# Performance work log

Hardware: AMD Instinct MI355X
Metric: run time of the kernel (lower is better)

Reference implementation:

```python
import jax, jax.numpy as jnp
import numpy as np

NUM_EXPERTS = 64
TOP_K = 2
NOISE_EPS = 0.01


def setup_inputs() -> dict:
    key = jax.random.key(0)
    k1, k2, k3, k4 = jax.random.split(key, 4)
    B, D, E = 32768, 2048, NUM_EXPERTS
    x = jax.random.normal(k1, (B, D), dtype=jnp.float32)
    # original inits these to zero; use small random weights for a non-degenerate top-k
    w_gate = jax.random.normal(k2, (D, E), dtype=jnp.float32) * 0.02
    w_noise = jax.random.normal(k3, (D, E), dtype=jnp.float32) * 0.02
    noise = jax.random.normal(k4, (B, E), dtype=jnp.float32)  # tf.random.normal draw, fixed
    return {"x": x, "w_gate": w_gate, "w_noise": w_noise, "noise": noise}


def reference(x, w_gate, w_noise, noise):
    # routing_pooling='flatten' on a 2D input is identity
    pooled = x  # [B, D]
    routing = pooled @ w_gate  # [B, E]
    # noisy routing (training=True path)
    noise_stddev = jax.nn.softplus(pooled @ w_noise) + NOISE_EPS
    routing = routing + noise * noise_stddev
    # softmax_top_k: take top k+1, keep top k, softmax, scatter back to E experts
    kk = min(TOP_K + 1, NUM_EXPERTS)
    top_vals, top_idx = jax.lax.top_k(routing, kk)
    top_k_vals = top_vals[:, :TOP_K]            # [B, k]
    top_k_idx = top_idx[:, :TOP_K]              # [B, k]
    top_k_gates = jax.nn.softmax(top_k_vals, axis=-1)
    B = routing.shape[0]
    rows = jnp.arange(B)[:, None]
    # rowwise_unsorted_segment_sum -> scatter gates into expert slots
    out = jnp.zeros((B, NUM_EXPERTS), dtype=routing.dtype).at[rows, top_k_idx].add(top_k_gates)
    return out
```

## Files before the change

kernel.cpp:

```cpp
#include <hip/hip_runtime.h>
#include <math.h>


typedef _Float16 half8v __attribute__((ext_vector_type(8)));
typedef float f32x4  __attribute__((ext_vector_type(4)));
typedef float f32x16 __attribute__((ext_vector_type(16)));

constexpr int DIMK = 2048;
constexpr int NEXP = 64;
constexpr int BM   = 64;
constexpr int NCH  = DIMK / 32;

__device__ __forceinline__ void async_load16(const void* g, void* l) {
    __builtin_amdgcn_global_load_lds(
        (const __attribute__((address_space(1))) unsigned int*)g,
        (__attribute__((address_space(3))) unsigned int*)l, 16, 0, 0);
}

__device__ __forceinline__ bool gt_pair(float a, int ia, float b, int ib) {
    return (a > b) || (a == b && ia < ib);
}

__global__ __launch_bounds__(256)
void presplit_kernel(const float* __restrict__ wg, const float* __restrict__ wn,
                     _Float16* __restrict__ wsB)
{
    int gid  = blockIdx.x * 256 + threadIdx.x;
    int lane = gid & 63;
    int fb   = gid >> 6;
    int nt   = fb & 3;
    int p    = (fb >> 2) & 1;
    int kh   = (fb >> 3) & 1;
    int c    = fb >> 4;
    const float* src = (nt < 2) ? (wg + nt * 32 + (lane & 31))
                                : (wn + (nt - 2) * 32 + (lane & 31));
    int kb = c * 32 + kh * 16 + ((lane >> 5) << 3);
    half8v hp;
    #pragma unroll
    for (int j = 0; j < 8; ++j) {
        float w = src[(size_t)(kb + j) * NEXP] * 65536.0f;
        _Float16 a = (_Float16)w;
        hp[j] = p ? (_Float16)(w - (float)a) : a;
    }
    *(half8v*)(wsB + (size_t)fb * 512 + lane * 8) = hp;
}

__global__ __launch_bounds__(256, 2)
void routing_mfma(const float* __restrict__ x, const _Float16* __restrict__ wsB,
                  const float* __restrict__ noise, float* __restrict__ out)
{
    __shared__ _Float16 Bp[4][16][64][8];
    __shared__ float4   cand[BM][2];
    __shared__ float4   res[BM];

    const int tid  = threadIdx.x;
    const int lane = tid & 63;
    const int w    = tid >> 6;
    const int rg   = w >> 1;
    const int colh = w & 1;
    const int m    = lane & 31;
    const int h    = lane >> 5;
    const int row0 = blockIdx.x * BM;

    f32x16 acc[2] = {};
    float4 ra[4][4];
    half8v afH[2][2], afL[2][2];

    const float* xp = x + (size_t)(row0 + rg * 32 + m) * DIMK + h * 8;

    auto issue_B = [&](int c, int buf) {
        #pragma unroll
        for (int ii = 0; ii < 4; ++ii) {
            int idx = w * 4 + ii;
            const _Float16* g = wsB + ((size_t)c * 16 + idx) * 512 + lane * 8;
            async_load16(g, &Bp[buf][idx][0][0]);
        }
    };

#define ISSUE_X(C, S)                                            \
    {   const float* p_ = xp + (C) * 32;                         \
        ra[S][0] = *(const float4*)(p_);                         \
        ra[S][1] = *(const float4*)(p_ + 4);                     \
        ra[S][2] = *(const float4*)(p_ + 16);                    \
        ra[S][3] = *(const float4*)(p_ + 20);  }

#define CONVERT(C, P)                                                        \
    {   _Pragma("unroll")                                                    \
        for (int kh = 0; kh < 2; ++kh) {                                     \
            float4 u = ra[(C) & 3][kh * 2];                                  \
            float4 v = ra[(C) & 3][kh * 2 + 1];                              \
            float f0 = u.x * 1024.f, f1 = u.y * 1024.f;                      \
            float f2 = u.z * 1024.f, f3 = u.w * 1024.f;                      \
            float f4 = v.x * 1024.f, f5 = v.y * 1024.f;                      \
            float f6 = v.z * 1024.f, f7 = v.w * 1024.f;                      \
            _Float16 a0=(_Float16)f0, a1=(_Float16)f1, a2=(_Float16)f2,      \
                     a3=(_Float16)f3, a4=(_Float16)f4, a5=(_Float16)f5,      \
                     a6=(_Float16)f6, a7=(_Float16)f7;                       \
            afH[P][kh][0]=a0; afH[P][kh][1]=a1; afH[P][kh][2]=a2;            \
            afH[P][kh][3]=a3; afH[P][kh][4]=a4; afH[P][kh][5]=a5;            \
            afH[P][kh][6]=a6; afH[P][kh][7]=a7;                             \
            afL[P][kh][0]=(_Float16)(f0-(float)a0);                         \
            afL[P][kh][1]=(_Float16)(f1-(float)a1);                         \
            afL[P][kh][2]=(_Float16)(f2-(float)a2);                         \
            afL[P][kh][3]=(_Float16)(f3-(float)a3);                         \
            afL[P][kh][4]=(_Float16)(f4-(float)a4);                         \
            afL[P][kh][5]=(_Float16)(f5-(float)a5);                         \
            afL[P][kh][6]=(_Float16)(f6-(float)a6);                         \
            afL[P][kh][7]=(_Float16)(f7-(float)a7);                         \
        }                                                                    \
    }

#define FENCE() asm volatile("" ::: "memory")

#define STEP(T, ISS, CV, WN)                                                 \
    {                                                                        \
        asm volatile("s_waitcnt vmcnt(" #WN ")" ::: "memory");               \
        asm volatile("s_barrier" ::: "memory");                              \
        if (ISS) { issue_B((T) + 2, ((T) + 2) & 3);                          \
                   ISSUE_X((T) + 2, ((T) + 2) & 3); }                        \
        half8v bf[2][2][2];                                                  \
        _Pragma("unroll")                                                    \
        for (int kh = 0; kh < 2; ++kh)                                       \
            _Pragma("unroll")                                                \
            for (int p = 0; p < 2; ++p)                                      \
                _Pragma("unroll")                                            \
                for (int tl = 0; tl < 2; ++tl)                               \
                    bf[kh][p][tl] = *(const half8v*)                         \
                        &Bp[(T) & 3][kh * 8 + p * 4 + tl * 2 + colh][lane][0];\
        __builtin_amdgcn_s_setprio(1);                                       \
        _Pragma("unroll")                                                    \
        for (int tl = 0; tl < 2; ++tl)                                       \
            _Pragma("unroll")                                                \
            for (int kh = 0; kh < 2; ++kh) {                                 \
                acc[tl] = __builtin_amdgcn_mfma_f32_32x32x16_f16(            \
                    afH[(T) & 1][kh], bf[kh][0][tl], acc[tl], 0, 0, 0);      \
                acc[tl] = __builtin_amdgcn_mfma_f32_32x32x16_f16(            \
                    afH[(T) & 1][kh], bf[kh][1][tl], acc[tl], 0, 0, 0);      \
                acc[tl] = __builtin_amdgcn_mfma_f32_32x32x16_f16(            \
                    afL[(T) & 1][kh], bf[kh][0][tl], acc[tl], 0, 0, 0);      \
            }                                                                \
        __builtin_amdgcn_s_setprio(0);                                       \
        if (CV) CONVERT((T) + 1, ((T) + 1) & 1);                             \
    }

    issue_B(0, 0);
    ISSUE_X(0, 0);
    FENCE();
    issue_B(1, 1);
    ISSUE_X(1, 1);
    CONVERT(0, 0);

    #pragma unroll 1
    for (int t = 0; t < NCH - 4; t += 4) {
        STEP(t + 0, 1, 1, 8)
        STEP(t + 1, 1, 1, 8)
        STEP(t + 2, 1, 1, 8)
        STEP(t + 3, 1, 1, 8)
    }
    STEP(NCH - 4, 1, 1, 8)
    STEP(NCH - 3, 1, 1, 8)
    STEP(NCH - 2, 0, 1, 8)
    STEP(NCH - 1, 0, 0, 0)

#undef STEP
#undef CONVERT
#undef ISSUE_X
#undef FENCE

    const float s = 0x1p-26f;
    {
        const int e = colh * 32 + m;
        #pragma unroll
        for (int reg = 0; reg < 16; ++reg) {
            int r    = (reg & 3) + 8 * (reg >> 2) + 4 * h;
            int grow = row0 + rg * 32 + r;
            float nz   = noise[(size_t)grow * NEXP + e];
            float gate = acc[0][reg] * s;
            float nv   = acc[1][reg] * s;
            float sp   = fmaxf(nv, 0.f) + log1pf(expf(-fabsf(nv)));
            float vv   = gate + nz * (sp + 0.01f);
            float v1 = vv; int i1 = e;
            float v2 = -INFINITY; int i2 = 0x7fffffff;
            #pragma unroll
            for (int mm = 1; mm <= 16; mm <<= 1) {
                float b1 = __shfl_xor(v1, mm); int ib1 = __shfl_xor(i1, mm);
                float b2 = __shfl_xor(v2, mm); int ib2 = __shfl_xor(i2, mm);
                if (gt_pair(b1, ib1, v1, i1)) {
                    float o1 = v1; int oi1 = i1;
                    v1 = b1; i1 = ib1;
                    if (gt_pair(b2, ib2, o1, oi1)) { v2 = b2; i2 = ib2; }
                    else                           { v2 = o1; i2 = oi1; }
                } else if (gt_pair(b1, ib1, v2, i2)) {
                    v2 = b1; i2 = ib1;
                }
            }
            if (m == 0)
                cand[rg * 32 + r][colh] = make_float4(v1, __int_as_float(i1),
                                                      v2, __int_as_float(i2));
        }
    }
    __syncthreads();

    if (tid < BM) {
        float4 c0 = cand[tid][0], c1 = cand[tid][1];
        float mv1 = c0.x; int mi1 = __float_as_int(c0.y);
        float mv2 = c0.z; int mi2 = __float_as_int(c0.w);
        float b1 = c1.x;  int ib1 = __float_as_int(c1.y);
        float b2 = c1.z;  int ib2 = __float_as_int(c1.w);
        if (gt_pair(b1, ib1, mv1, mi1)) {
            float o1 = mv1; int oi1 = mi1;
            mv1 = b1; mi1 = ib1;
            if (gt_pair(b2, ib2, o1, oi1)) { mv2 = b2; mi2 = ib2; }
            else                           { mv2 = o1; mi2 = oi1; }
        } else if (gt_pair(b1, ib1, mv2, mi2)) {
            mv2 = b1; mi2 = ib1;
        }
        float t  = expf(mv2 - mv1);
        float g1 = 1.f / (1.f + t);
        res[tid] = make_float4(g1, __int_as_float(mi1),
                               t * g1, __int_as_float(mi2));
    }
    __syncthreads();

    {
        int rr  = tid >> 2;
        int seg = tid & 3;
        float4 rv = res[rr];
        float g1 = rv.x, g2 = rv.z;
        int   j1 = __float_as_int(rv.y), j2 = __float_as_int(rv.w);
        float* op = out + (size_t)(row0 + rr) * NEXP + seg * 16;
        #pragma unroll
        for (int qq = 0; qq < 4; ++qq) {
            int e0 = seg * 16 + qq * 4;
            float4 o;
            o.x = (e0 + 0 == j1) ? g1 : ((e0 + 0 == j2) ? g2 : 0.f);
            o.y = (e0 + 1 == j1) ? g1 : ((e0 + 1 == j2) ? g2 : 0.f);
            o.z = (e0 + 2 == j1) ? g1 : ((e0 + 2 == j2) ? g2 : 0.f);
            o.w = (e0 + 3 == j1) ? g1 : ((e0 + 3 == j2) ? g2 : 0.f);
            *(float4*)(op + qq * 4) = o;
        }
    }
}

extern "C" void kernel_launch(void* const* d_in, const int* in_sizes, int n_in,
                              void* d_out, int out_size, void* d_ws, size_t ws_size,
                              hipStream_t stream) {
    const float* x     = (const float*)d_in[0];
    const float* wg    = (const float*)d_in[1];
    const float* wn    = (const float*)d_in[2];
    const float* noise = (const float*)d_in[3];
    float* out = (float*)d_out;
    _Float16* wsB = (_Float16*)d_ws;

    presplit_kernel<<<dim3(256), 256, 0, stream>>>(wg, wn, wsB);

    const int Brows = in_sizes[0] / DIMK;
    dim3 grid(Brows / BM);
    routing_mfma<<<grid, 256, 0, stream>>>(x, wsB, noise, out);
}
```

Measured before the change: 435.8 us.

## Shrink row tile to 32 with per-wave private B buffers and no barriers

Halves the row tile to 32 rows per block and gives each wave its own 32-column slice of the weight operand in a private LDS region, so the main loop no longer needs block-wide barriers. The x-to-fp16 hi/lo conversion now happens inline in each step rather than one step ahead, and the buffering drops from four stages to two. The epilogue stages accumulators through LDS and does the top-2 selection per row across 8 threads with fewer shuffles. Each block does less work with more blocks resident per CU, but each wave now loads the same x rows redundantly, and the inline conversion may leave the MFMA pipe less well fed.

```diff
diff --git a/kernel.cpp b/kernel.cpp
--- a/kernel.cpp
+++ b/kernel.cpp
@@ -8,7 +8,7 @@
 
 constexpr int DIMK = 2048;
 constexpr int NEXP = 64;
-constexpr int BM   = 64;
+constexpr int BM   = 32;
 constexpr int NCH  = DIMK / 32;
 
 __device__ __forceinline__ void async_load16(const void* g, void* l) {
@@ -45,36 +45,34 @@
     *(half8v*)(wsB + (size_t)fb * 512 + lane * 8) = hp;
 }
 
-__global__ __launch_bounds__(256, 2)
+__global__ __launch_bounds__(256, 4)
 void routing_mfma(const float* __restrict__ x, const _Float16* __restrict__ wsB,
                   const float* __restrict__ noise, float* __restrict__ out)
 {
-    __shared__ _Float16 Bp[4][16][64][8];
-    __shared__ float4   cand[BM][2];
+    __shared__ _Float16 Bp[4][2][4][64][8];
     __shared__ float4   res[BM];
 
     const int tid  = threadIdx.x;
     const int lane = tid & 63;
     const int w    = tid >> 6;
-    const int rg   = w >> 1;
-    const int colh = w & 1;
     const int m    = lane & 31;
     const int h    = lane >> 5;
     const int row0 = blockIdx.x * BM;
 
-    f32x16 acc[2] = {};
-    float4 ra[4][4];
-    half8v afH[2][2], afL[2][2];
-
-    const float* xp = x + (size_t)(row0 + rg * 32 + m) * DIMK + h * 8;
+    f32x16 acc = {};
+    float4 ra[2][4];
+
+    const float* xp = x + (size_t)(row0 + m) * DIMK + h * 8;
 
     auto issue_B = [&](int c, int buf) {
         #pragma unroll
-        for (int ii = 0; ii < 4; ++ii) {
-            int idx = w * 4 + ii;
-            const _Float16* g = wsB + ((size_t)c * 16 + idx) * 512 + lane * 8;
-            async_load16(g, &Bp[buf][idx][0][0]);
-        }
+        for (int kh = 0; kh < 2; ++kh)
+            #pragma unroll
+            for (int p = 0; p < 2; ++p) {
+                int fb = c * 16 + kh * 8 + p * 4 + w;
+                async_load16(wsB + (size_t)fb * 512 + lane * 8,
+                             &Bp[w][buf][kh * 2 + p][0][0]);
+            }
     };
 
 #define ISSUE_X(C, S)                                            \
@@ -84,11 +82,22 @@
         ra[S][2] = *(const float4*)(p_ + 16);                    \
         ra[S][3] = *(const float4*)(p_ + 20);  }
 
-#define CONVERT(C, P)                                                        \
-    {   _Pragma("unroll")                                                    \
+#define FENCE() asm volatile("" ::: "memory")
+
+#define STEP(C, SLOT, ISS, WN)                                               \
+    {                                                                        \
+        asm volatile("s_waitcnt vmcnt(" #WN ")" ::: "memory");               \
+        half8v bf[2][2];                                                     \
+        _Pragma("unroll")                                                    \
+        for (int kh = 0; kh < 2; ++kh)                                       \
+            _Pragma("unroll")                                                \
+            for (int p = 0; p < 2; ++p)                                      \
+                bf[kh][p] = *(const half8v*)&Bp[w][SLOT][kh * 2 + p][lane][0];\
+        half8v afH[2], afL[2];                                               \
+        _Pragma("unroll")                                                    \
         for (int kh = 0; kh < 2; ++kh) {                                     \
-            float4 u = ra[(C) & 3][kh * 2];                                  \
-            float4 v = ra[(C) & 3][kh * 2 + 1];                              \
+            float4 u = ra[SLOT][kh * 2];                                     \
+            float4 v = ra[SLOT][kh * 2 + 1];                                 \
             float f0 = u.x * 1024.f, f1 = u.y * 1024.f;                      \
             float f2 = u.z * 1024.f, f3 = u.w * 1024.f;                      \
             float f4 = v.x * 1024.f, f5 = v.y * 1024.f;                      \
@@ -96,51 +105,30 @@
             _Float16 a0=(_Float16)f0, a1=(_Float16)f1, a2=(_Float16)f2,      \
                      a3=(_Float16)f3, a4=(_Float16)f4, a5=(_Float16)f5,      \
                      a6=(_Float16)f6, a7=(_Float16)f7;                       \
-            afH[P][kh][0]=a0; afH[P][kh][1]=a1; afH[P][kh][2]=a2;            \
-            afH[P][kh][3]=a3; afH[P][kh][4]=a4; afH[P][kh][5]=a5;            \
-            afH[P][kh][6]=a6; afH[P][kh][7]=a7;                             \
-            afL[P][kh][0]=(_Float16)(f0-(float)a0);                         \
-            afL[P][kh][1]=(_Float16)(f1-(float)a1);                         \
-            afL[P][kh][2]=(_Float16)(f2-(float)a2);                         \
-            afL[P][kh][3]=(_Float16)(f3-(float)a3);                         \
-            afL[P][kh][4]=(_Float16)(f4-(float)a4);                         \
-            afL[P][kh][5]=(_Float16)(f5-(float)a5);                         \
-            afL[P][kh][6]=(_Float16)(f6-(float)a6);                         \
-            afL[P][kh][7]=(_Float16)(f7-(float)a7);                         \
+            afH[kh][0]=a0; afH[kh][1]=a1; afH[kh][2]=a2; afH[kh][3]=a3;      \
+            afH[kh][4]=a4; afH[kh][5]=a5; afH[kh][6]=a6; afH[kh][7]=a7;      \
+            afL[kh][0]=(_Float16)(f0-(float)a0);                             \
+            afL[kh][1]=(_Float16)(f1-(float)a1);                             \
+            afL[kh][2]=(_Float16)(f2-(float)a2);                             \
+            afL[kh][3]=(_Float16)(f3-(float)a3);                             \
+            afL[kh][4]=(_Float16)(f4-(float)a4);                             \
+            afL[kh][5]=(_Float16)(f5-(float)a5);                             \
+            afL[kh][6]=(_Float16)(f6-(float)a6);                             \
+            afL[kh][7]=(_Float16)(f7-(float)a7);                             \
         }                                                                    \
-    }
-
-#define FENCE() asm volatile("" ::: "memory")
-
-#define STEP(T, ISS, CV, WN)                                                 \
-    {                                                                        \
-        asm volatile("s_waitcnt vmcnt(" #WN ")" ::: "memory");               \
-        asm volatile("s_barrier" ::: "memory");                              \
-        if (ISS) { issue_B((T) + 2, ((T) + 2) & 3);                          \
-                   ISSUE_X((T) + 2, ((T) + 2) & 3); }                        \
-        half8v bf[2][2][2];                                                  \
-        _Pragma("unroll")                                                    \
-        for (int kh = 0; kh < 2; ++kh)                                       \
-            _Pragma("unroll")                                                \
-            for (int p = 0; p < 2; ++p)                                      \
-                _Pragma("unroll")                                            \
-                for (int tl = 0; tl < 2; ++tl)                               \
-                    bf[kh][p][tl] = *(const half8v*)                         \
-                        &Bp[(T) & 3][kh * 8 + p * 4 + tl * 2 + colh][lane][0];\
+        asm volatile("s_waitcnt lgkmcnt(0)" ::: "memory");                   \
+        if (ISS) { issue_B((C) + 2, SLOT); ISSUE_X((C) + 2, SLOT); }         \
         __builtin_amdgcn_s_setprio(1);                                       \
         _Pragma("unroll")                                                    \
-        for (int tl = 0; tl < 2; ++tl)                                       \
-            _Pragma("unroll")                                                \
-            for (int kh = 0; kh < 2; ++kh) {                                 \
-                acc[tl] = __builtin_amdgcn_mfma_f32_32x32x16_f16(            \
-                    afH[(T) & 1][kh], bf[kh][0][tl], acc[tl], 0, 0, 0);      \
-                acc[tl] = __builtin_amdgcn_mfma_f32_32x32x16_f16(            \
-                    afH[(T) & 1][kh], bf[kh][1][tl], acc[tl], 0, 0, 0);      \
-                acc[tl] = __builtin_amdgcn_mfma_f32_32x32x16_f16(            \
-                    afL[(T) & 1][kh], bf[kh][0][tl], acc[tl], 0, 0, 0);      \
-            }                                                                \
+        for (int kh = 0; kh < 2; ++kh) {                                     \
+            acc = __builtin_amdgcn_mfma_f32_32x32x16_f16(                    \
+                afH[kh], bf[kh][0], acc, 0, 0, 0);                           \
+            acc = __builtin_amdgcn_mfma_f32_32x32x16_f16(                    \
+                afH[kh], bf[kh][1], acc, 0, 0, 0);                           \
+            acc = __builtin_amdgcn_mfma_f32_32x32x16_f16(                    \
+                afL[kh], bf[kh][0], acc, 0, 0, 0);                           \
+        }                                                                    \
         __builtin_amdgcn_s_setprio(0);                                       \
-        if (CV) CONVERT((T) + 1, ((T) + 1) & 1);                             \
     }
 
     issue_B(0, 0);
@@ -148,90 +136,84 @@
     FENCE();
     issue_B(1, 1);
     ISSUE_X(1, 1);
-    CONVERT(0, 0);
 
     #pragma unroll 1
-    for (int t = 0; t < NCH - 4; t += 4) {
-        STEP(t + 0, 1, 1, 8)
-        STEP(t + 1, 1, 1, 8)
-        STEP(t + 2, 1, 1, 8)
-        STEP(t + 3, 1, 1, 8)
-    }
-    STEP(NCH - 4, 1, 1, 8)
+    for (int c = 0; c < NCH - 4; c += 2) {
+        STEP(c + 0, 0, 1, 8)
+        STEP(c + 1, 1, 1, 8)
+    }
+    STEP(NCH - 4, 0, 1, 8)
     STEP(NCH - 3, 1, 1, 8)
-    STEP(NCH - 2, 0, 1, 8)
-    STEP(NCH - 1, 0, 0, 0)
+    STEP(NCH - 2, 0, 0, 8)
+    STEP(NCH - 1, 1, 0, 0)
 
 #undef STEP
-#undef CONVERT
 #undef ISSUE_X
 #undef FENCE
 
     const float s = 0x1p-26f;
     {
-        const int e = colh * 32 + m;
+        float* scr = (float*)&Bp[w][0][0][0][0];
         #pragma unroll
         for (int reg = 0; reg < 16; ++reg) {
-            int r    = (reg & 3) + 8 * (reg >> 2) + 4 * h;
-            int grow = row0 + rg * 32 + r;
-            float nz   = noise[(size_t)grow * NEXP + e];
-            float gate = acc[0][reg] * s;
-            float nv   = acc[1][reg] * s;
+            int r = (reg & 3) + 8 * (reg >> 2) + 4 * h;
+            scr[r * 33 + m] = acc[reg] * s;
+        }
+    }
+    __syncthreads();
+
+    {
+        int r  = tid >> 3;
+        int s8 = tid & 7;
+        const float* gsrc = (const float*)&Bp[s8 >> 2][0][0][0][0];
+        const float* nsrc = (const float*)&Bp[2 + (s8 >> 2)][0][0][0][0];
+        int cs = (s8 * 8) & 31;
+        float4 z0 = *(const float4*)(noise + (size_t)(row0 + r) * NEXP + s8 * 8);
+        float4 z1 = *(const float4*)(noise + (size_t)(row0 + r) * NEXP + s8 * 8 + 4);
+        float zz[8] = {z0.x, z0.y, z0.z, z0.w, z1.x, z1.y, z1.z, z1.w};
+        float v1 = -INFINITY, v2 = -INFINITY; int i1 = 0x7ffffffe, i2 = 0x7fffffff;
+        #pragma unroll
+        for (int j = 0; j < 8; ++j) {
+            float gate = gsrc[r * 33 + cs + j];
+            float nv   = nsrc[r * 33 + cs + j];
             float sp   = fmaxf(nv, 0.f) + log1pf(expf(-fabsf(nv)));
-            float vv   = gate + nz * (sp + 0.01f);
-            float v1 = vv; int i1 = e;
-            float v2 = -INFINITY; int i2 = 0x7fffffff;
-            #pragma unroll
-            for (int mm = 1; mm <= 16; mm <<= 1) {
-                float b1 = __shfl_xor(v1, mm); int ib1 = __shfl_xor(i1, mm);
-                float b2 = __shfl_xor(v2, mm); int ib2 = __shfl_xor(i2, mm);
-                if (gt_pair(b1, ib1, v1, i1)) {
-                    float o1 = v1; int oi1 = i1;
-                    v1 = b1; i1 = ib1;
-                    if (gt_pair(b2, ib2, o1, oi1)) { v2 = b2; i2 = ib2; }
-                    else                           { v2 = o1; i2 = oi1; }
-                } else if (gt_pair(b1, ib1, v2, i2)) {
-                    v2 = b1; i2 = ib1;
-                }
+            float vv   = gate + zz[j] * (sp + 0.01f);
+            int   e    = s8 * 8 + j;
+            if (gt_pair(vv, e, v1, i1)) { v2 = v1; i2 = i1; v1 = vv; i1 = e; }
+            else if (gt_pair(vv, e, v2, i2)) { v2 = vv; i2 = e; }
+        }
+        #pragma unroll
+        for (int mm = 1; mm <= 4; mm <<= 1) {
+            float b1 = __shfl_xor(v1, mm); int ib1 = __shfl_xor(i1, mm);
+            float b2 = __shfl_xor(v2, mm); int ib2 = __shfl_xor(i2, mm);
+            if (gt_pair(b1, ib1, v1, i1)) {
+                float o1 = v1; int oi1 = i1;
+                v1 = b1; i1 = ib1;
+                if (gt_pair(b2, ib2, o1, oi1)) { v2 = b2; i2 = ib2; }
+                else                           { v2 = o1; i2 = oi1; }
+            } else if (gt_pair(b1, ib1, v2, i2)) {
+                v2 = b1; i2 = ib1;
             }
-            if (m == 0)
-                cand[rg * 32 + r][colh] = make_float4(v1, __int_as_float(i1),
-                                                      v2, __int_as_float(i2));
+        }
+        if (s8 == 0) {
+            float t  = expf(v2 - v1);
+            float g1 = 1.f / (1.f + t);
+            res[r] = make_float4(g1, __int_as_float(i1),
+                                 t * g1, __int_as_float(i2));
         }
     }
     __syncthreads();
 
-    if (tid < BM) {
-        float4 c0 = cand[tid][0], c1 = cand[tid][1];
-        float mv1 = c0.x; int mi1 = __float_as_int(c0.y);
-        float mv2 = c0.z; int mi2 = __float_as_int(c0.w);
-        float b1 = c1.x;  int ib1 = __float_as_int(c1.y);
-        float b2 = c1.z;  int ib2 = __float_as_int(c1.w);
-        if (gt_pair(b1, ib1, mv1, mi1)) {
-            float o1 = mv1; int oi1 = mi1;
-            mv1 = b1; mi1 = ib1;
-            if (gt_pair(b2, ib2, o1, oi1)) { mv2 = b2; mi2 = ib2; }
-            else                           { mv2 = o1; mi2 = oi1; }
-        } else if (gt_pair(b1, ib1, mv2, mi2)) {
-            mv2 = b1; mi2 = ib1;
-        }
-        float t  = expf(mv2 - mv1);
-        float g1 = 1.f / (1.f + t);
-        res[tid] = make_float4(g1, __int_as_float(mi1),
-                               t * g1, __int_as_float(mi2));
-    }
-    __syncthreads();
-
     {
-        int rr  = tid >> 2;
-        int seg = tid & 3;
+        int rr  = tid >> 3;
+        int seg = tid & 7;
         float4 rv = res[rr];
         float g1 = rv.x, g2 = rv.z;
         int   j1 = __float_as_int(rv.y), j2 = __float_as_int(rv.w);
-        float* op = out + (size_t)(row0 + rr) * NEXP + seg * 16;
-        #pragma unroll
-        for (int qq = 0; qq < 4; ++qq) {
-            int e0 = seg * 16 + qq * 4;
+        float* op = out + (size_t)(row0 + rr) * NEXP + seg * 8;
+        #pragma unroll
+        for (int qq = 0; qq < 2; ++qq) {
+            int e0 = seg * 8 + qq * 4;
             float4 o;
             o.x = (e0 + 0 == j1) ? g1 : ((e0 + 0 == j2) ? g2 : 0.f);
             o.y = (e0 + 1 == j1) ? g1 : ((e0 + 1 == j2) ? g2 : 0.f);
```

Result: slower. 472.9 us (+8.5%).
